# Kernel optimization log

Measured on AMD Instinct MI355X. Metric: run time of the kernel, lower is better.

The kernel has to match this reference:

```python
import jax, jax.numpy as jnp
import numpy as np

B, LQ, LA, H = 32, 1024, 1024, 512
NEG_INF = jnp.float32(-1e7)  # matches torch masked_fill_(-10000000.0)


def setup_inputs() -> dict:
    key = jax.random.key(0)
    k1, k2, k3, k4 = jax.random.split(key, 4)
    q = jax.random.normal(k1, (B, LQ, H), dtype=jnp.float32)
    a = jax.random.normal(k2, (B, LA, H), dtype=jnp.float32)
    q_mask = jax.random.randint(k3, (B, LQ, 1), 0, 2).astype(jnp.int32)
    a_mask = jax.random.randint(k4, (B, LA, 1), 0, 2).astype(jnp.int32)
    # learned scalar, initialized exactly as in __init__
    temperature = jnp.float32(1.0 / np.sqrt(H))
    return {"q": q, "a": a, "q_mask": q_mask, "a_mask": a_mask,
            "temperature": temperature}


def reference(q, a, q_mask, a_mask, temperature):
    # scaled co-attention scores: [B, Lq, La]
    attn = jnp.einsum('bqh,bah->bqa', q, a) * temperature
    # validity mask via outer product of per-token masks (nonzero = valid)
    mask = jnp.matmul(q_mask.astype(jnp.float32),
                      a_mask.transpose(0, 2, 1).astype(jnp.float32)) != 0
    attn = jnp.where(mask, attn, NEG_INF)
    # dual-axis softmax over the SAME score matrix
    attn_q = jax.nn.softmax(attn, axis=1)  # normalize over Lq
    attn_a = jax.nn.softmax(attn, axis=2)  # normalize over La
    # aggregation: a_s = attn_q^T @ q -> [B, La, H]; q_s = attn_a @ a -> [B, Lq, H]
    a_s = jnp.einsum('bqa,bqh->bah', attn_q, q)
    q_s = jnp.einsum('bqa,bah->bqh', attn_a, a)
    return (jnp.concatenate([q, q_s], axis=-1),
            jnp.concatenate([a, a_s], axis=-1))
```

## Files before the change

kernel.cpp:

```cpp
#include <hip/hip_runtime.h>
#include <cstdint>
#include <cstddef>

#define NB   32
#define LQA  1024
#define HD   512

typedef __attribute__((ext_vector_type(4))) float  f32x4;
typedef __attribute__((ext_vector_type(8))) short  s16x8;
typedef __attribute__((ext_vector_type(4))) unsigned short u16x4;

static __device__ __forceinline__ unsigned short f2bf(float f) {
  unsigned int u = __builtin_bit_cast(unsigned int, f);
  u += 0x7fffu + ((u >> 16) & 1u);
  return (unsigned short)(u >> 16);
}
static __device__ __forceinline__ float bf2f(unsigned short h) {
  unsigned int u = ((unsigned int)h) << 16;
  return __builtin_bit_cast(float, u);
}
static __device__ __forceinline__ u16x4 cvt4(f32x4 v) {
  u16x4 r;
  r.x = f2bf(v.x); r.y = f2bf(v.y); r.z = f2bf(v.z); r.w = f2bf(v.w);
  return r;
}

typedef __attribute__((address_space(1))) const void gas_void;
typedef __attribute__((address_space(3))) void las_void;
static __device__ __forceinline__ void gload_lds16(const void* g, void* l) {
  __builtin_amdgcn_global_load_lds((gas_void*)g, (las_void*)l, 16, 0, 0);
}

__global__ __launch_bounds__(256) void k_transpose_copy(
    const float* __restrict__ src,
    float* __restrict__ out_left,
    unsigned short* __restrict__ dstT,
    unsigned short* __restrict__ dstN)
{
  const int b  = blockIdx.z;
  const int h0 = blockIdx.x * 64;
  const int q0 = blockIdx.y * 64;
  const int t  = threadIdx.x;

  __shared__ unsigned short T[64 * 68];

  const float* sb = src + (size_t)b * LQA * HD;
  float* ob       = out_left + (size_t)b * LQA * 1024;
  unsigned short* db  = dstT + (size_t)b * HD * LQA;
  unsigned short* dbn = dstN + (size_t)b * LQA * HD;

#pragma unroll
  for (int j = 0; j < 4; ++j) {
    int f = t + 256 * j;
    int r = f >> 4;
    int c = (f & 15) * 4;
    f32x4 v = *(const f32x4*)(sb + (size_t)(q0 + r) * HD + h0 + c);
    *(f32x4*)(ob + (size_t)(q0 + r) * 1024 + h0 + c) = v;
    u16x4 cv = cvt4(v);
    *(u16x4*)&dbn[(size_t)(q0 + r) * HD + h0 + c] = cv;
    *(u16x4*)&T[r * 68 + c] = cv;
  }
  __syncthreads();
#pragma unroll
  for (int j = 0; j < 4; ++j) {
    int f = t + 256 * j;
    int orow = f >> 4;
    int c = (f & 15) * 4;
    u16x4 v;
    v.x = T[(c + 0) * 68 + orow];
    v.y = T[(c + 1) * 68 + orow];
    v.z = T[(c + 2) * 68 + orow];
    v.w = T[(c + 3) * 68 + orow];
    *(u16x4*)&db[(size_t)(h0 + orow) * LQA + q0 + c] = v;
  }
}

__global__ __launch_bounds__(256) void k_scores(
    const unsigned short* __restrict__ qb16, const unsigned short* __restrict__ ab16,
    const int* __restrict__ qmask, const int* __restrict__ amask,
    const float* __restrict__ temp_p,
    unsigned short* __restrict__ E, unsigned short* __restrict__ ET,
    float* __restrict__ rowsumE,
    float* __restrict__ colsumE)
{
  const int flat = blockIdx.x;
  const int xcd  = flat & 7;
  const int i5   = flat >> 3;
  const int b    = (i5 >> 6) * 8 + xcd;
  const int tile = i5 & 63;
  const int m0 = (tile & 7) * 128;
  const int n0 = (tile >> 3) * 128;

  const int t  = threadIdx.x;
  const int lane = t & 63;
  const int w  = t >> 6;
  const int moff = (w & 1) * 64;
  const int noff = (w >> 1) * 64;
  const int lrow = lane & 15;
  const int quad = lane >> 4;

  __shared__ __align__(16) unsigned short smem[128 * 132];
  unsigned short* As = smem;
  unsigned short* Bs = smem + 4096;

  const unsigned short* qb = qb16 + (size_t)b * LQA * HD;
  const unsigned short* ab = ab16 + (size_t)b * LQA * HD;

  const int fa = t, fb = t + 256;
  const unsigned short* qg0 = qb + (size_t)(m0 + (fa >> 2)) * HD + (fa & 3) * 8;
  const unsigned short* qg1 = qb + (size_t)(m0 + (fb >> 2)) * HD + (fb & 3) * 8;
  const unsigned short* ag0 = ab + (size_t)(n0 + (fa >> 2)) * HD + (fa & 3) * 8;
  const unsigned short* ag1 = ab + (size_t)(n0 + (fb >> 2)) * HD + (fb & 3) * 8;
  unsigned short* As0 = As + w * 512;
  unsigned short* As1 = As + (4 + w) * 512;
  unsigned short* Bs0 = Bs + w * 512;
  unsigned short* Bs1 = Bs + (4 + w) * 512;

  f32x4 acc[4][4];
#pragma unroll
  for (int i = 0; i < 4; ++i)
#pragma unroll
    for (int j = 0; j < 4; ++j) acc[i][j] = (f32x4)0.f;

  for (int kt = 0; kt < HD / 32; ++kt) {
    const int ko = kt * 32;
    gload_lds16(qg0 + ko, As0);
    gload_lds16(qg1 + ko, As1);
    gload_lds16(ag0 + ko, Bs0);
    gload_lds16(ag1 + ko, Bs1);
    __syncthreads();
    s16x8 af[4], bfr[4];
#pragma unroll
    for (int i = 0; i < 4; ++i) {
      af[i]  = *(const s16x8*)&As[(moff + i * 16 + lrow) * 32 + quad * 8];
      bfr[i] = *(const s16x8*)&Bs[(noff + i * 16 + lrow) * 32 + quad * 8];
    }
#pragma unroll
    for (int i = 0; i < 4; ++i)
#pragma unroll
      for (int j = 0; j < 4; ++j)
        acc[i][j] = __builtin_amdgcn_mfma_f32_16x16x32_bf16(af[i], bfr[j], acc[i][j], 0, 0, 0);
    __syncthreads();
  }

  unsigned short* Cs = smem;
  const float temp = temp_p[0];
  const int* qmb = qmask + b * LQA;
  const int* amb = amask + b * LQA;

  float rowp[4][4];
  float colp[4];
#pragma unroll
  for (int i = 0; i < 4; ++i)
#pragma unroll
    for (int r = 0; r < 4; ++r) rowp[i][r] = 0.f;
#pragma unroll
  for (int j = 0; j < 4; ++j) colp[j] = 0.f;

#pragma unroll
  for (int i = 0; i < 4; ++i) {
#pragma unroll
    for (int j = 0; j < 4; ++j) {
      int ncol = noff + j * 16 + lrow;
      float am = (amb[n0 + ncol] != 0) ? 1.f : 0.f;
#pragma unroll
      for (int r = 0; r < 4; ++r) {
        int mrow = moff + i * 16 + quad * 4 + r;
        float qm = (qmb[m0 + mrow] != 0) ? 1.f : 0.f;
        float e = __expf(acc[i][j][r] * temp) * am * qm;
        unsigned short eb = f2bf(e);
        float er = bf2f(eb);
        Cs[mrow * 132 + ncol] = eb;
        rowp[i][r] += er;
        colp[j] += er;
      }
    }
  }

#pragma unroll
  for (int i = 0; i < 4; ++i)
#pragma unroll
    for (int r = 0; r < 4; ++r) {
      float v = rowp[i][r];
      v += __shfl_xor(v, 1); v += __shfl_xor(v, 2);
      v += __shfl_xor(v, 4); v += __shfl_xor(v, 8);
      if (lrow == 0)
        atomicAdd(&rowsumE[(size_t)b * LQA + m0 + moff + i * 16 + quad * 4 + r], v);
    }
#pragma unroll
  for (int j = 0; j < 4; ++j) {
    float v = colp[j];
    v += __shfl_xor(v, 16); v += __shfl_xor(v, 32);
    if (quad == 0)
      atomicAdd(&colsumE[(size_t)b * LQA + n0 + noff + j * 16 + lrow], v);
  }

  __syncthreads();
  const size_t Ebase = (size_t)b * LQA * LQA;
#pragma unroll
  for (int jj = 0; jj < 16; ++jj) {
    int f = t + 256 * jj;
    int row = f >> 5;
    int c = (f & 31) * 4;
    u16x4 v = *(const u16x4*)&Cs[row * 132 + c];
    *(u16x4*)&E[Ebase + (size_t)(m0 + row) * LQA + n0 + c] = v;
  }
#pragma unroll
  for (int jj = 0; jj < 16; ++jj) {
    int f = t + 256 * jj;
    int orow = f >> 5;
    int c = (f & 31) * 4;
    u16x4 v;
    v.x = Cs[(c + 0) * 132 + orow];
    v.y = Cs[(c + 1) * 132 + orow];
    v.z = Cs[(c + 2) * 132 + orow];
    v.w = Cs[(c + 3) * 132 + orow];
    *(u16x4*)&ET[Ebase + (size_t)(n0 + orow) * LQA + m0 + c] = v;
  }
}

__global__ __launch_bounds__(256) void k_rowsum_plain(
    const unsigned short* __restrict__ M, float* __restrict__ sums)
{
  const int t = threadIdx.x;
  const int rowg = blockIdx.x * 16 + (t >> 4);
  const int s = t & 15;
  const unsigned short* rp = M + (size_t)rowg * LQA;
  float sum = 0.f;
#pragma unroll
  for (int it = 0; it < 16; ++it) {
    u16x4 v = *(const u16x4*)&rp[it * 64 + s * 4];
    sum += bf2f(v.x) + bf2f(v.y) + bf2f(v.z) + bf2f(v.w);
  }
  sum += __shfl_xor(sum, 1);
  sum += __shfl_xor(sum, 2);
  sum += __shfl_xor(sum, 4);
  sum += __shfl_xor(sum, 8);
  if (s == 0) sums[rowg] = sum;
}

__global__ __launch_bounds__(256) void k_stats(
    const float* __restrict__ sums, float2* __restrict__ invadd)
{
  const int idx = blockIdx.x * 256 + threadIdx.x;
  float s = sums[idx];
  float2 o;
  if (s > 0.f) { o.x = 1.f / s; o.y = 0.f; }
  else         { o.x = 0.f;     o.y = 1.f / 1024.f; }
  invadd[idx] = o;
}

__global__ __launch_bounds__(256) void k_agg(
    const unsigned short* __restrict__ Emat,
    const unsigned short* __restrict__ Bt,
    const float2* __restrict__ invadd,
    const float* __restrict__ bsum,
    float* __restrict__ outp)
{
  const int flat = blockIdx.x;
  const int xcd  = flat & 7;
  const int i5   = flat >> 3;
  const int b    = (i5 >> 5) * 8 + xcd;
  const int tile = i5 & 31;
  const int m0 = (tile & 7) * 128;
  const int n0 = (tile >> 3) * 128;

  const int t  = threadIdx.x;
  const int lane = t & 63;
  const int w  = t >> 6;
  const int moff = (w & 1) * 64;
  const int noff = (w >> 1) * 64;
  const int lrow = lane & 15;
  const int quad = lane >> 4;

  __shared__ __align__(16) unsigned short As[128 * 32];
  __shared__ __align__(16) unsigned short Bs[128 * 32];

  const unsigned short* Eb = Emat + (size_t)b * LQA * LQA;
  const unsigned short* Bb = Bt + (size_t)b * HD * LQA;

  const int fa = t, fb = t + 256;
  const unsigned short* eg0 = Eb + (size_t)(m0 + (fa >> 2)) * LQA + (fa & 3) * 8;
  const unsigned short* eg1 = Eb + (size_t)(m0 + (fb >> 2)) * LQA + (fb & 3) * 8;
  const unsigned short* bg0 = Bb + (size_t)(n0 + (fa >> 2)) * LQA + (fa & 3) * 8;
  const unsigned short* bg1 = Bb + (size_t)(n0 + (fb >> 2)) * LQA + (fb & 3) * 8;
  unsigned short* As0 = As + w * 512;
  unsigned short* As1 = As + (4 + w) * 512;
  unsigned short* Bs0 = Bs + w * 512;
  unsigned short* Bs1 = Bs + (4 + w) * 512;

  f32x4 acc[4][4];
#pragma unroll
  for (int i = 0; i < 4; ++i)
#pragma unroll
    for (int j = 0; j < 4; ++j) acc[i][j] = (f32x4)0.f;

  for (int kt = 0; kt < LQA / 32; ++kt) {
    const int ko = kt * 32;
    gload_lds16(eg0 + ko, As0);
    gload_lds16(eg1 + ko, As1);
    gload_lds16(bg0 + ko, Bs0);
    gload_lds16(bg1 + ko, Bs1);
    __syncthreads();
    s16x8 af[4], bfr[4];
#pragma unroll
    for (int i = 0; i < 4; ++i) {
      af[i]  = *(const s16x8*)&As[(moff + i * 16 + lrow) * 32 + quad * 8];
      bfr[i] = *(const s16x8*)&Bs[(noff + i * 16 + lrow) * 32 + quad * 8];
    }
#pragma unroll
    for (int i = 0; i < 4; ++i)
#pragma unroll
      for (int j = 0; j < 4; ++j)
        acc[i][j] = __builtin_amdgcn_mfma_f32_16x16x32_bf16(af[i], bfr[j], acc[i][j], 0, 0, 0);
    __syncthreads();
  }

  const float2* ia = invadd + b * LQA;
  const float* bs = bsum + b * HD;
  float* ob = outp + (size_t)b * LQA * 1024;
#pragma unroll
  for (int i = 0; i < 4; ++i) {
#pragma unroll
    for (int j = 0; j < 4; ++j) {
      int ncol = noff + j * 16 + lrow;
      float bsv = bs[n0 + ncol];
#pragma unroll
      for (int r = 0; r < 4; ++r) {
        int mrow = moff + i * 16 + quad * 4 + r;
        float2 v = ia[m0 + mrow];
        ob[(size_t)(m0 + mrow) * 1024 + 512 + n0 + ncol] =
            v.x * acc[i][j][r] + v.y * bsv;
      }
    }
  }
}

extern "C" void kernel_launch(void* const* d_in, const int* in_sizes, int n_in,
                              void* d_out, int out_size, void* d_ws, size_t ws_size,
                              hipStream_t stream) {
  (void)in_sizes; (void)n_in; (void)out_size; (void)ws_size;
  const float* q    = (const float*)d_in[0];
  const float* a    = (const float*)d_in[1];
  const int*   qm   = (const int*)d_in[2];
  const int*   am   = (const int*)d_in[3];
  const float* temp = (const float*)d_in[4];

  float* out0 = (float*)d_out;
  float* out1 = out0 + (size_t)NB * LQA * 1024;

  char* ws = (char*)d_ws;
  const size_t MB = 1024ull * 1024ull;
  unsigned short* E    = (unsigned short*)(ws);
  unsigned short* ET   = (unsigned short*)(ws + 64 * MB);
  unsigned short* qT   = (unsigned short*)(ws + 128 * MB);
  unsigned short* aT   = (unsigned short*)(ws + 160 * MB);
  unsigned short* qb16 = (unsigned short*)(ws + 192 * MB);
  unsigned short* ab16 = (unsigned short*)(ws + 224 * MB);
  float*  sums  = (float*)(ws + 256 * MB);
  float2* invadd= (float2*)(ws + 256 * MB + (256 << 10));
  float*  qsum  = (float*)(ws + 256 * MB + (768 << 10));
  float*  asum  = (float*)(ws + 256 * MB + (832 << 10));

  k_transpose_copy<<<dim3(8, 16, NB), 256, 0, stream>>>(q, out0, qT, qb16);
  k_transpose_copy<<<dim3(8, 16, NB), 256, 0, stream>>>(a, out1, aT, ab16);
  hipMemsetAsync(sums, 0, (size_t)2 * NB * LQA * sizeof(float), stream);
  k_rowsum_plain<<<dim3(NB * HD / 16), 256, 0, stream>>>(qT, qsum);
  k_rowsum_plain<<<dim3(NB * HD / 16), 256, 0, stream>>>(aT, asum);
  k_scores<<<dim3(2048), 256, 0, stream>>>(qb16, ab16, qm, am, temp,
                                           E, ET, sums, sums + NB * LQA);
  k_stats<<<dim3(2 * NB * LQA / 256), 256, 0, stream>>>(sums, invadd);
  k_agg<<<dim3(1024), 256, 0, stream>>>(E,  aT, invadd,            asum, out0);
  k_agg<<<dim3(1024), 256, 0, stream>>>(ET, qT, invadd + NB * LQA, qsum, out1);
}
```

Before: 608.8 us.

## Fuse prep, column sums and stats into fewer kernels and widen K tiles

Merges the two transpose/convert kernels into one launch and computes the per-H column sums inside it with shuffles plus atomics, which removes the separate rowsum kernels. The stats kernel is folded into the aggregation epilogue, and the two aggregation launches become a single 2048-block launch. Both GEMM loops now stage a K depth of 64 per barrier instead of 32, halving the number of syncs at the cost of twice the LDS per block. Atomics add some contention, and the larger LDS footprint may lower occupancy.

New measurement: 616.7 us. About the same (+1.3%).

```diff
diff --git a/kernel.cpp b/kernel.cpp
--- a/kernel.cpp
+++ b/kernel.cpp
@@ -31,16 +31,25 @@
   __builtin_amdgcn_global_load_lds((gas_void*)g, (las_void*)l, 16, 0, 0);
 }
 
-__global__ __launch_bounds__(256) void k_transpose_copy(
-    const float* __restrict__ src,
-    float* __restrict__ out_left,
-    unsigned short* __restrict__ dstT,
-    unsigned short* __restrict__ dstN)
+__global__ __launch_bounds__(256) void k_prep(
+    const float* __restrict__ qsrc, const float* __restrict__ asrc,
+    float* __restrict__ out0, float* __restrict__ out1,
+    unsigned short* __restrict__ qT, unsigned short* __restrict__ aT,
+    unsigned short* __restrict__ qb16, unsigned short* __restrict__ ab16,
+    float* __restrict__ qsum, float* __restrict__ asum)
 {
-  const int b  = blockIdx.z;
+  const int bz  = blockIdx.z;
+  const int isA = bz >> 5;
+  const int b   = bz & 31;
   const int h0 = blockIdx.x * 64;
   const int q0 = blockIdx.y * 64;
   const int t  = threadIdx.x;
+
+  const float* src = isA ? asrc : qsrc;
+  float* out_left      = isA ? out1 : out0;
+  unsigned short* dstT = isA ? aT : qT;
+  unsigned short* dstN = isA ? ab16 : qb16;
+  float* csum          = isA ? asum : qsum;
 
   __shared__ unsigned short T[64 * 68];
 
@@ -72,6 +81,11 @@
     v.z = T[(c + 2) * 68 + orow];
     v.w = T[(c + 3) * 68 + orow];
     *(u16x4*)&db[(size_t)(h0 + orow) * LQA + q0 + c] = v;
+    float s = bf2f(v.x) + bf2f(v.y) + bf2f(v.z) + bf2f(v.w);
+    s += __shfl_xor(s, 1); s += __shfl_xor(s, 2);
+    s += __shfl_xor(s, 4); s += __shfl_xor(s, 8);
+    if ((t & 15) == 0)
+      atomicAdd(&csum[(size_t)b * HD + h0 + orow], s);
   }
 }
 
@@ -101,20 +115,13 @@
 
   __shared__ __align__(16) unsigned short smem[128 * 132];
   unsigned short* As = smem;
-  unsigned short* Bs = smem + 4096;
+  unsigned short* Bs = smem + 8192;
 
   const unsigned short* qb = qb16 + (size_t)b * LQA * HD;
   const unsigned short* ab = ab16 + (size_t)b * LQA * HD;
 
-  const int fa = t, fb = t + 256;
-  const unsigned short* qg0 = qb + (size_t)(m0 + (fa >> 2)) * HD + (fa & 3) * 8;
-  const unsigned short* qg1 = qb + (size_t)(m0 + (fb >> 2)) * HD + (fb & 3) * 8;
-  const unsigned short* ag0 = ab + (size_t)(n0 + (fa >> 2)) * HD + (fa & 3) * 8;
-  const unsigned short* ag1 = ab + (size_t)(n0 + (fb >> 2)) * HD + (fb & 3) * 8;
-  unsigned short* As0 = As + w * 512;
-  unsigned short* As1 = As + (4 + w) * 512;
-  unsigned short* Bs0 = Bs + w * 512;
-  unsigned short* Bs1 = Bs + (4 + w) * 512;
+  const unsigned short* qg = qb + (size_t)(m0 + (t >> 3)) * HD + (t & 7) * 8;
+  const unsigned short* ag = ab + (size_t)(n0 + (t >> 3)) * HD + (t & 7) * 8;
 
   f32x4 acc[4][4];
 #pragma unroll
@@ -122,24 +129,28 @@
 #pragma unroll
     for (int j = 0; j < 4; ++j) acc[i][j] = (f32x4)0.f;
 
-  for (int kt = 0; kt < HD / 32; ++kt) {
-    const int ko = kt * 32;
-    gload_lds16(qg0 + ko, As0);
-    gload_lds16(qg1 + ko, As1);
-    gload_lds16(ag0 + ko, Bs0);
-    gload_lds16(ag1 + ko, Bs1);
+  for (int kt = 0; kt < HD / 64; ++kt) {
+    const int ko = kt * 64;
+#pragma unroll
+    for (int p = 0; p < 4; ++p) {
+      gload_lds16(qg + ko + p * 32 * HD, As + (w + 4 * p) * 512);
+      gload_lds16(ag + ko + p * 32 * HD, Bs + (w + 4 * p) * 512);
+    }
     __syncthreads();
-    s16x8 af[4], bfr[4];
-#pragma unroll
-    for (int i = 0; i < 4; ++i) {
-      af[i]  = *(const s16x8*)&As[(moff + i * 16 + lrow) * 32 + quad * 8];
-      bfr[i] = *(const s16x8*)&Bs[(noff + i * 16 + lrow) * 32 + quad * 8];
-    }
-#pragma unroll
-    for (int i = 0; i < 4; ++i)
-#pragma unroll
-      for (int j = 0; j < 4; ++j)
-        acc[i][j] = __builtin_amdgcn_mfma_f32_16x16x32_bf16(af[i], bfr[j], acc[i][j], 0, 0, 0);
+#pragma unroll
+    for (int ks = 0; ks < 2; ++ks) {
+      s16x8 af[4], bfr[4];
+#pragma unroll
+      for (int i = 0; i < 4; ++i) {
+        af[i]  = *(const s16x8*)&As[(moff + i * 16 + lrow) * 64 + ks * 32 + quad * 8];
+        bfr[i] = *(const s16x8*)&Bs[(noff + i * 16 + lrow) * 64 + ks * 32 + quad * 8];
+      }
+#pragma unroll
+      for (int i = 0; i < 4; ++i)
+#pragma unroll
+        for (int j = 0; j < 4; ++j)
+          acc[i][j] = __builtin_amdgcn_mfma_f32_16x16x32_bf16(af[i], bfr[j], acc[i][j], 0, 0, 0);
+    }
     __syncthreads();
   }
 
@@ -219,51 +230,31 @@
   }
 }
 
-__global__ __launch_bounds__(256) void k_rowsum_plain(
-    const unsigned short* __restrict__ M, float* __restrict__ sums)
+__global__ __launch_bounds__(256) void k_agg2(
+    const unsigned short* __restrict__ Ein,
+    const unsigned short* __restrict__ ETin,
+    const unsigned short* __restrict__ qT,
+    const unsigned short* __restrict__ aT,
+    const float* __restrict__ sums,
+    const float* __restrict__ qsum,
+    const float* __restrict__ asum,
+    float* __restrict__ out0, float* __restrict__ out1)
 {
-  const int t = threadIdx.x;
-  const int rowg = blockIdx.x * 16 + (t >> 4);
-  const int s = t & 15;
-  const unsigned short* rp = M + (size_t)rowg * LQA;
-  float sum = 0.f;
-#pragma unroll
-  for (int it = 0; it < 16; ++it) {
-    u16x4 v = *(const u16x4*)&rp[it * 64 + s * 4];
-    sum += bf2f(v.x) + bf2f(v.y) + bf2f(v.z) + bf2f(v.w);
-  }
-  sum += __shfl_xor(sum, 1);
-  sum += __shfl_xor(sum, 2);
-  sum += __shfl_xor(sum, 4);
-  sum += __shfl_xor(sum, 8);
-  if (s == 0) sums[rowg] = sum;
-}
-
-__global__ __launch_bounds__(256) void k_stats(
-    const float* __restrict__ sums, float2* __restrict__ invadd)
-{
-  const int idx = blockIdx.x * 256 + threadIdx.x;
-  float s = sums[idx];
-  float2 o;
-  if (s > 0.f) { o.x = 1.f / s; o.y = 0.f; }
-  else         { o.x = 0.f;     o.y = 1.f / 1024.f; }
-  invadd[idx] = o;
-}
-
-__global__ __launch_bounds__(256) void k_agg(
-    const unsigned short* __restrict__ Emat,
-    const unsigned short* __restrict__ Bt,
-    const float2* __restrict__ invadd,
-    const float* __restrict__ bsum,
-    float* __restrict__ outp)
-{
-  const int flat = blockIdx.x;
-  const int xcd  = flat & 7;
-  const int i5   = flat >> 3;
+  const int flat  = blockIdx.x;
+  const int half  = flat >> 10;
+  const int inner = flat & 1023;
+  const int xcd  = inner & 7;
+  const int i5   = inner >> 3;
   const int b    = (i5 >> 5) * 8 + xcd;
   const int tile = i5 & 31;
   const int m0 = (tile & 7) * 128;
   const int n0 = (tile >> 3) * 128;
+
+  const unsigned short* Emat = half ? ETin : Ein;
+  const unsigned short* Bt   = half ? qT : aT;
+  const float* srow = sums + (size_t)half * NB * LQA + (size_t)b * LQA;
+  const float* bsp  = (half ? qsum : asum) + (size_t)b * HD;
+  float* ob = (half ? out1 : out0) + (size_t)b * LQA * 1024;
 
   const int t  = threadIdx.x;
   const int lane = t & 63;
@@ -273,21 +264,14 @@
   const int lrow = lane & 15;
   const int quad = lane >> 4;
 
-  __shared__ __align__(16) unsigned short As[128 * 32];
-  __shared__ __align__(16) unsigned short Bs[128 * 32];
+  __shared__ __align__(16) unsigned short As[128 * 64];
+  __shared__ __align__(16) unsigned short Bs[128 * 64];
 
   const unsigned short* Eb = Emat + (size_t)b * LQA * LQA;
   const unsigned short* Bb = Bt + (size_t)b * HD * LQA;
 
-  const int fa = t, fb = t + 256;
-  const unsigned short* eg0 = Eb + (size_t)(m0 + (fa >> 2)) * LQA + (fa & 3) * 8;
-  const unsigned short* eg1 = Eb + (size_t)(m0 + (fb >> 2)) * LQA + (fb & 3) * 8;
-  const unsigned short* bg0 = Bb + (size_t)(n0 + (fa >> 2)) * LQA + (fa & 3) * 8;
-  const unsigned short* bg1 = Bb + (size_t)(n0 + (fb >> 2)) * LQA + (fb & 3) * 8;
-  unsigned short* As0 = As + w * 512;
-  unsigned short* As1 = As + (4 + w) * 512;
-  unsigned short* Bs0 = Bs + w * 512;
-  unsigned short* Bs1 = Bs + (4 + w) * 512;
+  const unsigned short* eg = Eb + (size_t)(m0 + (t >> 3)) * LQA + (t & 7) * 8;
+  const unsigned short* bg = Bb + (size_t)(n0 + (t >> 3)) * LQA + (t & 7) * 8;
 
   f32x4 acc[4][4];
 #pragma unroll
@@ -295,42 +279,47 @@
 #pragma unroll
     for (int j = 0; j < 4; ++j) acc[i][j] = (f32x4)0.f;
 
-  for (int kt = 0; kt < LQA / 32; ++kt) {
-    const int ko = kt * 32;
-    gload_lds16(eg0 + ko, As0);
-    gload_lds16(eg1 + ko, As1);
-    gload_lds16(bg0 + ko, Bs0);
-    gload_lds16(bg1 + ko, Bs1);
+  for (int kt = 0; kt < LQA / 64; ++kt) {
+    const int ko = kt * 64;
+#pragma unroll
+    for (int p = 0; p < 4; ++p) {
+      gload_lds16(eg + ko + p * 32 * LQA, As + (w + 4 * p) * 512);
+      gload_lds16(bg + ko + p * 32 * LQA, Bs + (w + 4 * p) * 512);
+    }
     __syncthreads();
-    s16x8 af[4], bfr[4];
-#pragma unroll
-    for (int i = 0; i < 4; ++i) {
-      af[i]  = *(const s16x8*)&As[(moff + i * 16 + lrow) * 32 + quad * 8];
-      bfr[i] = *(const s16x8*)&Bs[(noff + i * 16 + lrow) * 32 + quad * 8];
-    }
-#pragma unroll
-    for (int i = 0; i < 4; ++i)
-#pragma unroll
-      for (int j = 0; j < 4; ++j)
-        acc[i][j] = __builtin_amdgcn_mfma_f32_16x16x32_bf16(af[i], bfr[j], acc[i][j], 0, 0, 0);
+#pragma unroll
+    for (int ks = 0; ks < 2; ++ks) {
+      s16x8 af[4], bfr[4];
+#pragma unroll
+      for (int i = 0; i < 4; ++i) {
+        af[i]  = *(const s16x8*)&As[(moff + i * 16 + lrow) * 64 + ks * 32 + quad * 8];
+        bfr[i] = *(const s16x8*)&Bs[(noff + i * 16 + lrow) * 64 + ks * 32 + quad * 8];
+      }
+#pragma unroll
+      for (int i = 0; i < 4; ++i)
+#pragma unroll
+        for (int j = 0; j < 4; ++j)
+          acc[i][j] = __builtin_amdgcn_mfma_f32_16x16x32_bf16(af[i], bfr[j], acc[i][j], 0, 0, 0);
+    }
     __syncthreads();
   }
 
-  const float2* ia = invadd + b * LQA;
-  const float* bs = bsum + b * HD;
-  float* ob = outp + (size_t)b * LQA * 1024;
+  float bcol[4];
+#pragma unroll
+  for (int j = 0; j < 4; ++j) bcol[j] = bsp[n0 + noff + j * 16 + lrow];
 #pragma unroll
   for (int i = 0; i < 4; ++i) {
 #pragma unroll
-    for (int j = 0; j < 4; ++j) {
-      int ncol = noff + j * 16 + lrow;
-      float bsv = bs[n0 + ncol];
-#pragma unroll
-      for (int r = 0; r < 4; ++r) {
-        int mrow = moff + i * 16 + quad * 4 + r;
-        float2 v = ia[m0 + mrow];
+    for (int r = 0; r < 4; ++r) {
+      int mrow = moff + i * 16 + quad * 4 + r;
+      float s = srow[m0 + mrow];
+      float inv = (s > 0.f) ? 1.f / s : 0.f;
+      float add = (s > 0.f) ? 0.f : (1.f / 1024.f);
+#pragma unroll
+      for (int j = 0; j < 4; ++j) {
+        int ncol = noff + j * 16 + lrow;
         ob[(size_t)(m0 + mrow) * 1024 + 512 + n0 + ncol] =
-            v.x * acc[i][j][r] + v.y * bsv;
+            inv * acc[i][j][r] + add * bcol[j];
       }
     }
   }
@@ -357,19 +346,15 @@
   unsigned short* aT   = (unsigned short*)(ws + 160 * MB);
   unsigned short* qb16 = (unsigned short*)(ws + 192 * MB);
   unsigned short* ab16 = (unsigned short*)(ws + 224 * MB);
-  float*  sums  = (float*)(ws + 256 * MB);
-  float2* invadd= (float2*)(ws + 256 * MB + (256 << 10));
-  float*  qsum  = (float*)(ws + 256 * MB + (768 << 10));
-  float*  asum  = (float*)(ws + 256 * MB + (832 << 10));
-
-  k_transpose_copy<<<dim3(8, 16, NB), 256, 0, stream>>>(q, out0, qT, qb16);
-  k_transpose_copy<<<dim3(8, 16, NB), 256, 0, stream>>>(a, out1, aT, ab16);
-  hipMemsetAsync(sums, 0, (size_t)2 * NB * LQA * sizeof(float), stream);
-  k_rowsum_plain<<<dim3(NB * HD / 16), 256, 0, stream>>>(qT, qsum);
-  k_rowsum_plain<<<dim3(NB * HD / 16), 256, 0, stream>>>(aT, asum);
+  float* sums = (float*)(ws + 256 * MB);
+  float* qsum = (float*)(ws + 256 * MB + (256 << 10));
+  float* asum = (float*)(ws + 256 * MB + (320 << 10));
+
+  hipMemsetAsync(sums, 0, (size_t)(2 * NB * LQA + 2 * NB * HD) * sizeof(float), stream);
+  k_prep<<<dim3(8, 16, 2 * NB), 256, 0, stream>>>(q, a, out0, out1, qT, aT,
+                                                  qb16, ab16, qsum, asum);
   k_scores<<<dim3(2048), 256, 0, stream>>>(qb16, ab16, qm, am, temp,
                                            E, ET, sums, sums + NB * LQA);
-  k_stats<<<dim3(2 * NB * LQA / 256), 256, 0, stream>>>(sums, invadd);
-  k_agg<<<dim3(1024), 256, 0, stream>>>(E,  aT, invadd,            asum, out0);
-  k_agg<<<dim3(1024), 256, 0, stream>>>(ET, qT, invadd + NB * LQA, qsum, out1);
-}
+  k_agg2<<<dim3(2048), 256, 0, stream>>>(E, ET, qT, aT, sums, qsum, asum,
+                                         out0, out1);
+}
```
